# Kernel tuning notes

Measured on AMD Instinct MI355X. Metric: run time of the kernel, lower is better.

Reference implementation:

```python
import jax, jax.numpy as jnp
import numpy as np

B, N, E, H, Z = 8, 10000, 160000, 128, 64

def setup_inputs() -> dict:
    key = jax.random.key(0)
    ks = jax.random.split(key, 12)
    def w(k, shape):
        fan_in = shape[-1]
        return (jax.random.uniform(k, shape, jnp.float32, -1.0, 1.0) / np.sqrt(fan_in)).astype(jnp.float32)
    return {
        "x_node": jax.random.normal(ks[0], (B, N), jnp.float32),
        "edge_index": jax.random.randint(ks[1], (2, E), 0, N, dtype=jnp.int64),
        # layer 1: SAGEConv(1 -> H)
        "W1l": w(ks[2], (H, 1)), "b1": jnp.zeros((H,), jnp.float32), "W1r": w(ks[3], (H, 1)),
        # layer 2: SAGEConv(H -> H)
        "W2l": w(ks[4], (H, H)), "b2": jnp.zeros((H,), jnp.float32), "W2r": w(ks[5], (H, H)),
        # readout MLP: Linear(H,H) -> ReLU -> Linear(H,Z)
        "Wro1": w(ks[6], (H, H)), "bro1": jnp.zeros((H,), jnp.float32),
        "Wro2": w(ks[7], (Z, H)), "bro2": jnp.zeros((Z,), jnp.float32),
    }

def _sage_conv(h, src, dst, n_nodes, Wl, bl, Wr):
    """h: (B, N, din). out_i = Wl @ mean_{j->i} h_j + bl + Wr @ h_i."""
    msg = h[:, src, :]  # (B, E, din) gather from source nodes
    agg_sum = jax.vmap(lambda m: jax.ops.segment_sum(m, dst, num_segments=n_nodes))(msg)  # (B, N, din)
    deg = jax.ops.segment_sum(jnp.ones(dst.shape, h.dtype), dst, num_segments=n_nodes)  # (N,)
    agg = agg_sum / jnp.maximum(deg, 1.0)[None, :, None]  # mean; 0 for isolated nodes
    return jnp.einsum('bnd,hd->bnh', agg, Wl) + bl + jnp.einsum('bnd,hd->bnh', h, Wr)

def reference(x_node, edge_index, W1l, b1, W1r, W2l, b2, W2r, Wro1, bro1, Wro2, bro2):
    bsz, n = x_node.shape
    src, dst = edge_index[0], edge_index[1]
    h = x_node[:, :, None]  # (B, N, 1)
    h = jax.nn.relu(_sage_conv(h, src, dst, n, W1l, b1, W1r))
    h = jax.nn.relu(_sage_conv(h, src, dst, n, W2l, b2, W2r))
    pooled = jnp.mean(h, axis=1)  # global_mean_pool over nodes -> (B, H)
    hid = jax.nn.relu(pooled @ Wro1.T + bro1)
    return hid @ Wro2.T + bro2  # (B, Z)
```

## Files before the change

### kernel.cpp

```cpp
#include <hip/hip_runtime.h>
#include <hip/hip_bf16.h>

#define Bk 8
#define Nk 10000
#define Ek 160000
#define Hk 128
#define Zk 64
#define CAPk 64
#define NTILES 313
#define NROWS 10016

typedef float f32x4 __attribute__((ext_vector_type(4)));
typedef float f32x2 __attribute__((ext_vector_type(2)));
typedef short s16x8 __attribute__((ext_vector_type(8)));
typedef unsigned u32x4 __attribute__((ext_vector_type(4)));

__device__ inline f32x2 pk_add(f32x2 a, f32x2 b){
  f32x2 d; asm("v_pk_add_f32 %0, %1, %2" : "=v"(d) : "v"(a), "v"(b)); return d;
}
__device__ inline f32x2 bf2_to_f32x2(unsigned v){
  f32x2 r; r.x = __uint_as_float(v<<16); r.y = __uint_as_float(v & 0xffff0000u); return r;
}
__device__ inline unsigned pack_bf2(float lo, float hi){
  __hip_bfloat162 p; p.x = __float2bfloat16(lo); p.y = __float2bfloat16(hi);
  return *(unsigned*)&p;
}

__global__ __launch_bounds__(256) void k0_init(const float* __restrict__ W2l, const float* __restrict__ W2r,
                                               __hip_bfloat16* __restrict__ wbt, int* __restrict__ cur,
                                               float* __restrict__ pooled){
  int t = blockIdx.x*256 + threadIdx.x;
  if (t < 128*256){
    int o = t >> 8, k = t & 255;
    float v = (k < 128) ? W2l[o*128+k] : W2r[o*128+(k-128)];
    wbt[t] = __float2bfloat16(v);
  }
  if (t < Nk) cur[t] = 0;
  if (t < Bk*Hk) pooled[t] = 0.f;
}

__global__ void k3_fill(const int* __restrict__ ei, int* __restrict__ cur, int* __restrict__ csrsrc){
  int e = blockIdx.x*blockDim.x + threadIdx.x;
  if (e < Ek){
    int s = ei[e], d = ei[Ek+e];
    int p = atomicAdd(&cur[d], 1);
    if (p < CAPk) csrsrc[d*CAPk + p] = s;
  }
}

__global__ __launch_bounds__(256) void k45_h1(const float* __restrict__ x, const int* __restrict__ cur,
                        const int* __restrict__ csrsrc,
                        const float* __restrict__ W1l, const float* __restrict__ b1,
                        const float* __restrict__ W1r, __hip_bfloat16* __restrict__ h1){
  int i = blockIdx.x*4 + (threadIdx.x>>6);
  int lane = threadIdx.x & 63;
  if (i >= Nk){
    if (i < NROWS){
      #pragma unroll
      for (int b=0;b<Bk;b++)
        *(unsigned*)((void*)(h1 + ((size_t)b*NROWS + i)*128 + 2*lane)) = 0u;
    }
    return;
  }
  float2 wl = *(const float2*)(W1l + 2*lane);
  float2 wr = *(const float2*)(W1r + 2*lane);
  float2 bb = *(const float2*)(b1  + 2*lane);
  int degc = cur[i];
  int deg = min(degc, CAPk);
  const int* col = csrsrc + (size_t)i*CAPk;
  int j = 0;
  bool havej = (lane < deg);
  if (havej) j = col[lane];
  float inv = 1.f/fmaxf((float)degc, 1.f);

  float xx[Bk];
  #pragma unroll
  for (int b=0;b<Bk;b++){
    float v = 0.f;
    if (havej) v = x[b*Nk + j];
    xx[b] = v;
  }
  #pragma unroll
  for (int b=0;b<Bk;b++){
    float s = xx[b];
    s += __shfl_xor(s, 1);  s += __shfl_xor(s, 2);  s += __shfl_xor(s, 4);
    s += __shfl_xor(s, 8);  s += __shfl_xor(s, 16); s += __shfl_xor(s, 32);
    float a  = s * inv;
    float xi = x[b*Nk + i];
    float v0 = fmaxf(fmaf(a, wl.x, fmaf(xi, wr.x, bb.x)), 0.f);
    float v1 = fmaxf(fmaf(a, wl.y, fmaf(xi, wr.y, bb.y)), 0.f);
    *(unsigned*)((void*)(h1 + ((size_t)b*NROWS + i)*128 + 2*lane)) = pack_bf2(v0, v1);
  }
}

__device__ inline void mfma_bf16(f32x4& d, s16x8 a, s16x8 b){
  asm("v_mfma_f32_16x16x32_bf16 %0, %1, %2, %0" : "+v"(d) : "v"(a), "v"(b));
}

__global__ __launch_bounds__(256) void kB_fused(const __hip_bfloat16* __restrict__ h1,
                        const int* __restrict__ cur, const int* __restrict__ csrsrc,
                        const __hip_bfloat16* __restrict__ wbt, const float* __restrict__ b2,
                        float* __restrict__ pooled){
  __shared__ char At[32*512];
  __shared__ int scol[32*CAPk];
  __shared__ int sdeg[32];
  int b = blockIdx.x, tile = blockIdx.y;
  int tid = threadIdx.x;
  int wid = tid >> 6, lane = tid & 63;
  int g = lane >> 4, l4 = lane & 15;
  const __hip_bfloat16* h1b = h1 + (size_t)b*NROWS*128;

  if (tid < 32){
    int i = tile*32 + tid;
    sdeg[tid] = (i < Nk) ? cur[i] : 0;
  }
  __syncthreads();

  {
    const u32x4* src = (const u32x4*)(csrsrc + (size_t)tile*32*CAPk);
    u32x4* dst = (u32x4*)scol;
    #pragma unroll
    for (int h=0; h<2; ++h){
      int idx = h*256 + tid;
      u32x4 v = __builtin_nontemporal_load(src + idx);
      int row = idx >> 4;
      int p = (idx & 15) * 4;
      int d = min(sdeg[row], CAPk);
      if (p+0 >= d) v.x = Nk;
      if (p+1 >= d) v.y = Nk;
      if (p+2 >= d) v.z = Nk;
      if (p+3 >= d) v.w = Nk;
      dst[idx] = v;
    }
  }
  __syncthreads();

  #pragma unroll
  for (int c=0;c<2;c++){
    int rg = wid*8 + c*4 + g;
    int ig = tile*32 + rg;
    int dc = sdeg[rg];
    int d4 = (min(dc, CAPk) + 3) & ~3;
    int km = d4;
    km = max(km, __shfl_xor(km, 16));
    km = max(km, __shfl_xor(km, 32));

    u32x4 sv = *(const u32x4*)((const void*)(h1b + (size_t)ig*128 + l4*8));

    f32x2 a0={0.f,0.f}, a1={0.f,0.f}, a2={0.f,0.f}, a3={0.f,0.f};
    const int* colg = scol + rg*CAPk;
    #pragma unroll 2
    for (int k=0; k<km; ++k){
      int j = colg[k];
      u32x4 v = *(const u32x4*)((const void*)(h1b + (size_t)j*128 + l4*8));
      a0 = pk_add(a0, bf2_to_f32x2(v.x));
      a1 = pk_add(a1, bf2_to_f32x2(v.y));
      a2 = pk_add(a2, bf2_to_f32x2(v.z));
      a3 = pk_add(a3, bf2_to_f32x2(v.w));
    }
    float inv = 1.f/fmaxf((float)dc, 1.f);
    u32x4 outv;
    outv.x = pack_bf2(a0.x*inv, a0.y*inv);
    outv.y = pack_bf2(a1.x*inv, a1.y*inv);
    outv.z = pack_bf2(a2.x*inv, a2.y*inv);
    outv.w = pack_bf2(a3.x*inv, a3.y*inv);
    unsigned swz = (unsigned)((rg & 7) << 4);
    *(u32x4*)(At + rg*512 + ((unsigned)(l4*16) ^ swz))       = outv;
    *(u32x4*)(At + rg*512 + ((unsigned)(256 + l4*16) ^ swz)) = sv;
  }
  __syncthreads();

  int lr = lane & 15, lk = lane >> 4;
  f32x4 acc[2][2];
  #pragma unroll
  for (int mf=0; mf<2; ++mf)
    #pragma unroll
    for (int q=0; q<2; ++q) acc[mf][q] = (f32x4){0.f,0.f,0.f,0.f};

  unsigned rsw = (unsigned)((lr & 7) << 4);
  #pragma unroll
  for (int kk=0; kk<8; ++kk){
    unsigned cb = kk*64 + lk*16;
    s16x8 a0 = *(const s16x8*)(At + lr*512      + (cb ^ rsw));
    s16x8 a1 = *(const s16x8*)(At + (16+lr)*512 + (cb ^ rsw));
    #pragma unroll
    for (int q=0; q<2; ++q){
      int nf = wid*2 + q;
      s16x8 bfr = *(const s16x8*)(const void*)(wbt + (nf*16+lr)*256 + kk*32 + lk*8);
      mfma_bf16(acc[0][q], a0, bfr);
      mfma_bf16(acc[1][q], a1, bfr);
    }
  }

  #pragma unroll
  for (int q=0; q<2; ++q){
    int colc = (wid*2+q)*16 + lr;
    float bias = b2[colc];
    float v = 0.f;
    #pragma unroll
    for (int mf=0; mf<2; ++mf){
      int rbase = tile*32 + mf*16 + lk*4;
      #pragma unroll
      for (int r=0;r<4;++r){
        float val = fmaxf(acc[mf][q][r] + bias, 0.f);
        if (rbase + r < Nk) v += val;
      }
    }
    v += __shfl_xor(v, 16);
    v += __shfl_xor(v, 32);
    if (lane < 16) atomicAdd(&pooled[b*Hk + colc], v);
  }
}

__global__ void k7_final(const float* __restrict__ pooled, const float* __restrict__ Wro1,
                         const float* __restrict__ bro1, const float* __restrict__ Wro2,
                         const float* __restrict__ bro2, float* __restrict__ out){
  int b = blockIdx.x, t = threadIdx.x;
  __shared__ float pool[128];
  __shared__ float hid[128];
  pool[t] = pooled[b*Hk + t] * (1.0f/(float)Nk);
  __syncthreads();
  float s = bro1[t];
  for (int d=0; d<128; ++d) s += Wro1[t*128+d]*pool[d];
  hid[t] = fmaxf(s, 0.f);
  __syncthreads();
  if (t < Zk){
    float s2 = bro2[t];
    for (int d=0; d<128; ++d) s2 += Wro2[t*128+d]*hid[d];
    out[b*Zk + t] = s2;
  }
}

extern "C" void kernel_launch(void* const* d_in, const int* in_sizes, int n_in,
                              void* d_out, int out_size, void* d_ws, size_t ws_size,
                              hipStream_t stream) {
  const float* x    = (const float*)d_in[0];
  const int*   ei   = (const int*)d_in[1];
  const float* W1l  = (const float*)d_in[2];
  const float* b1   = (const float*)d_in[3];
  const float* W1r  = (const float*)d_in[4];
  const float* W2l  = (const float*)d_in[5];
  const float* b2   = (const float*)d_in[6];
  const float* W2r  = (const float*)d_in[7];
  const float* Wro1 = (const float*)d_in[8];
  const float* bro1 = (const float*)d_in[9];
  const float* Wro2 = (const float*)d_in[10];
  const float* bro2 = (const float*)d_in[11];
  float* out = (float*)d_out;

  char* ws = (char*)d_ws;
  int*   cur    = (int*)(ws + 0);
  float* pooled = (float*)(ws + 40448);
  __hip_bfloat16* wbt = (__hip_bfloat16*)(ws + 44544);
  int*   csrsrc = (int*)(ws + 110080);
  __hip_bfloat16* h1 = (__hip_bfloat16*)(ws + 2674176);

  k0_init<<<dim3(128), 256, 0, stream>>>(W2l, W2r, wbt, cur, pooled);
  k3_fill<<<dim3((Ek+255)/256), 256, 0, stream>>>(ei, cur, csrsrc);
  k45_h1<<<dim3(2504), 256, 0, stream>>>(x, cur, csrsrc, W1l, b1, W1r, h1);
  kB_fused<<<dim3(Bk, NTILES), 256, 0, stream>>>(h1, cur, csrsrc, wbt, b2, pooled);
  k7_final<<<dim3(Bk), 128, 0, stream>>>(pooled, Wro1, bro1, Wro2, bro2, out);
}
```

Before: 96.24 us.

## Pre-fill CSR padding with sentinel and read neighbor indices directly from global

The init kernel now writes the sentinel index Nk into every CSR slot (2504 blocks cover 641k ints, enough for 10016x64), so unused slots no longer need masking. The fused layer-2 kernel drops its shared-memory staging of column indices and the barrier that went with it. It reads neighbor indices as int4 straight from global memory and issues four gathered row loads per iteration, with 32-bit byte offsets. This trades a larger init write for less LDS traffic, one fewer sync, and more memory-level parallelism in the gather loop.

```diff
diff --git a/kernel.cpp b/kernel.cpp
--- a/kernel.cpp
+++ b/kernel.cpp
@@ -28,7 +28,7 @@
 
 __global__ __launch_bounds__(256) void k0_init(const float* __restrict__ W2l, const float* __restrict__ W2r,
                                                __hip_bfloat16* __restrict__ wbt, int* __restrict__ cur,
-                                               float* __restrict__ pooled){
+                                               float* __restrict__ pooled, int* __restrict__ csrsrc){
   int t = blockIdx.x*256 + threadIdx.x;
   if (t < 128*256){
     int o = t >> 8, k = t & 255;
@@ -37,6 +37,7 @@
   }
   if (t < Nk) cur[t] = 0;
   if (t < Bk*Hk) pooled[t] = 0.f;
+  csrsrc[t] = Nk;
 }
 
 __global__ void k3_fill(const int* __restrict__ ei, int* __restrict__ cur, int* __restrict__ csrsrc){
@@ -102,36 +103,17 @@
                         const __hip_bfloat16* __restrict__ wbt, const float* __restrict__ b2,
                         float* __restrict__ pooled){
   __shared__ char At[32*512];
-  __shared__ int scol[32*CAPk];
   __shared__ int sdeg[32];
   int b = blockIdx.x, tile = blockIdx.y;
   int tid = threadIdx.x;
   int wid = tid >> 6, lane = tid & 63;
   int g = lane >> 4, l4 = lane & 15;
-  const __hip_bfloat16* h1b = h1 + (size_t)b*NROWS*128;
+  const char* h1b = (const char*)(h1 + (size_t)b*NROWS*128);
+  unsigned loff = (unsigned)(l4*16);
 
   if (tid < 32){
     int i = tile*32 + tid;
     sdeg[tid] = (i < Nk) ? cur[i] : 0;
-  }
-  __syncthreads();
-
-  {
-    const u32x4* src = (const u32x4*)(csrsrc + (size_t)tile*32*CAPk);
-    u32x4* dst = (u32x4*)scol;
-    #pragma unroll
-    for (int h=0; h<2; ++h){
-      int idx = h*256 + tid;
-      u32x4 v = __builtin_nontemporal_load(src + idx);
-      int row = idx >> 4;
-      int p = (idx & 15) * 4;
-      int d = min(sdeg[row], CAPk);
-      if (p+0 >= d) v.x = Nk;
-      if (p+1 >= d) v.y = Nk;
-      if (p+2 >= d) v.z = Nk;
-      if (p+3 >= d) v.w = Nk;
-      dst[idx] = v;
-    }
   }
   __syncthreads();
 
@@ -145,18 +127,24 @@
     km = max(km, __shfl_xor(km, 16));
     km = max(km, __shfl_xor(km, 32));
 
-    u32x4 sv = *(const u32x4*)((const void*)(h1b + (size_t)ig*128 + l4*8));
+    u32x4 sv = *(const u32x4*)(h1b + (unsigned)(ig*256) + loff);
 
     f32x2 a0={0.f,0.f}, a1={0.f,0.f}, a2={0.f,0.f}, a3={0.f,0.f};
-    const int* colg = scol + rg*CAPk;
-    #pragma unroll 2
-    for (int k=0; k<km; ++k){
-      int j = colg[k];
-      u32x4 v = *(const u32x4*)((const void*)(h1b + (size_t)j*128 + l4*8));
-      a0 = pk_add(a0, bf2_to_f32x2(v.x));
-      a1 = pk_add(a1, bf2_to_f32x2(v.y));
-      a2 = pk_add(a2, bf2_to_f32x2(v.z));
-      a3 = pk_add(a3, bf2_to_f32x2(v.w));
+    const int* colg = csrsrc + ig*CAPk;
+    for (int k=0; k<km; k+=4){
+      int4 js = *(const int4*)(colg + k);
+      u32x4 v0 = *(const u32x4*)(h1b + (unsigned)(js.x*256) + loff);
+      u32x4 v1 = *(const u32x4*)(h1b + (unsigned)(js.y*256) + loff);
+      u32x4 v2 = *(const u32x4*)(h1b + (unsigned)(js.z*256) + loff);
+      u32x4 v3 = *(const u32x4*)(h1b + (unsigned)(js.w*256) + loff);
+      a0 = pk_add(a0, bf2_to_f32x2(v0.x)); a1 = pk_add(a1, bf2_to_f32x2(v0.y));
+      a2 = pk_add(a2, bf2_to_f32x2(v0.z)); a3 = pk_add(a3, bf2_to_f32x2(v0.w));
+      a0 = pk_add(a0, bf2_to_f32x2(v1.x)); a1 = pk_add(a1, bf2_to_f32x2(v1.y));
+      a2 = pk_add(a2, bf2_to_f32x2(v1.z)); a3 = pk_add(a3, bf2_to_f32x2(v1.w));
+      a0 = pk_add(a0, bf2_to_f32x2(v2.x)); a1 = pk_add(a1, bf2_to_f32x2(v2.y));
+      a2 = pk_add(a2, bf2_to_f32x2(v2.z)); a3 = pk_add(a3, bf2_to_f32x2(v2.w));
+      a0 = pk_add(a0, bf2_to_f32x2(v3.x)); a1 = pk_add(a1, bf2_to_f32x2(v3.y));
+      a2 = pk_add(a2, bf2_to_f32x2(v3.z)); a3 = pk_add(a3, bf2_to_f32x2(v3.w));
     }
     float inv = 1.f/fmaxf((float)dc, 1.f);
     u32x4 outv;
@@ -255,7 +243,7 @@
   int*   csrsrc = (int*)(ws + 110080);
   __hip_bfloat16* h1 = (__hip_bfloat16*)(ws + 2674176);
 
-  k0_init<<<dim3(128), 256, 0, stream>>>(W2l, W2r, wbt, cur, pooled);
+  k0_init<<<dim3(2504), 256, 0, stream>>>(W2l, W2r, wbt, cur, pooled, csrsrc);
   k3_fill<<<dim3((Ek+255)/256), 256, 0, stream>>>(ei, cur, csrsrc);
   k45_h1<<<dim3(2504), 256, 0, stream>>>(x, cur, csrsrc, W1l, b1, W1r, h1);
   kB_fused<<<dim3(Bk, NTILES), 256, 0, stream>>>(h1, cur, csrsrc, wbt, b2, pooled);
```

Result: faster. 87.08 us (-9.5%).
